# Kernel tuning notes

Measured on AMD Instinct MI355X. Metric: run time of the kernel, lower is better.

## Reference

```python
import jax, jax.numpy as jnp
import numpy as np
from jax.scipy.linalg import expm

ORDER = 256
SEQ_LEN = 4096
THETA = 4096.0
MEMORY_D = 4
INPUT_SIZE = 256
HIDDEN = 512
BATCH = 8


def _lmu_AB(order):
    # Continuous-time LMU (Legendre) state-space matrices
    q = np.arange(order, dtype=np.float64)
    r = 2.0 * q + 1.0
    i, j = np.meshgrid(q, q, indexing="ij")
    A = np.where(i < j, -1.0, (-1.0) ** (i - j + 1)) * r[:, None]
    B = ((-1.0) ** q * r)[:, None]
    return A, B


def _discretize_zoh(A, B, dt=1.0):
    # ZOH via augmented matrix exponential: expm([[A,B],[0,0]]*dt)
    n = A.shape[0]
    M = np.zeros((n + 1, n + 1))
    M[:n, :n] = A * dt
    M[:n, n:] = B * dt
    Md = expm(jnp.asarray(M, dtype=jnp.float64) if jax.config.jax_enable_x64 else jnp.asarray(M, dtype=jnp.float32))
    return Md[:n, :n].astype(jnp.float32), Md[:n, n:].astype(jnp.float32)


def _impulse_H(order, seq_len, theta):
    A, B = _lmu_AB(order)
    Ad, Bd = _discretize_zoh(A / theta, B / theta, 1.0)

    def step(A_i, _):
        # H_t = A^t B ; emit A_i @ Bd then advance A_i <- Ad @ A_i
        return Ad @ A_i, (A_i @ Bd)[:, 0]

    _, Hs = jax.lax.scan(step, jnp.eye(order, dtype=jnp.float32), None, length=seq_len)
    return Hs.T  # [order, seq_len]


def setup_inputs() -> dict:
    key = jax.random.key(0)
    k1, k2, k3, k4, k5 = jax.random.split(key, 5)
    x = jax.random.normal(k1, (BATCH, SEQ_LEN, INPUT_SIZE), dtype=jnp.float32)
    Wu_w = jax.random.normal(k2, (MEMORY_D, INPUT_SIZE), dtype=jnp.float32) * (1.0 / np.sqrt(INPUT_SIZE))
    Wu_b = jax.random.normal(k3, (MEMORY_D,), dtype=jnp.float32) * 0.01
    msz = MEMORY_D * ORDER + INPUT_SIZE
    Wh_w = jax.random.normal(k4, (HIDDEN, msz), dtype=jnp.float32) * (1.0 / np.sqrt(msz))
    Wh_b = jax.random.normal(k5, (HIDDEN,), dtype=jnp.float32) * 0.01
    H = _impulse_H(ORDER, SEQ_LEN, THETA)  # exact LMU impulse response buffer
    return {"x": x, "Wu_w": Wu_w, "Wu_b": Wu_b, "Wh_w": Wh_w, "Wh_b": Wh_b, "H": H}


def reference(x, Wu_w, Wu_b, Wh_w, Wh_b, H):
    B, L, _ = x.shape
    u = jax.nn.relu(x @ Wu_w.T + Wu_b)                     # [B, L, memory_d]
    fft_u = jnp.fft.rfft(u.transpose(0, 2, 1), n=2 * L, axis=-1)   # [B, md, L+1]
    fft_H = jnp.fft.rfft(H, n=2 * L, axis=-1)              # [order, L+1]
    temp = fft_u[:, :, None, :] * fft_H[None, None, :, :]  # [B, md, order, L+1]
    m = jnp.fft.irfft(temp, n=2 * L, axis=-1)[..., :L]     # [B, md, order, L]
    m = m.reshape(B, -1, L).transpose(0, 2, 1)             # [B, L, md*order]
    input_h = jnp.concatenate([m, x], axis=-1)             # [B, L, md*order + input]
    h = jax.nn.relu(input_h @ Wh_w.T + Wh_b)               # [B, L, hidden]
    return h, h[:, -1, :]
```

## Files before the change

kernel.cpp:

```cpp
#include <hip/hip_runtime.h>

#define NB 8
#define LSEQ 4096
#define INS 256
#define MD 4
#define ORD 256
#define HID 512
#define MSZ 1280
#define FS 4128
#define NSPEC 8256
#define GMT 1056768
#define GNT 16384

#define PD(n) ((n) + ((n) >> 3))
#define LDSN 4608

typedef __attribute__((ext_vector_type(8))) short short8;
typedef __attribute__((ext_vector_type(4))) float floatx4;

struct ush4 { unsigned short x, y, z, w; };

__device__ float2 g_tw4096[4096];
__device__ float2 g_tw8192[4098];

__device__ __forceinline__ unsigned short f2bf(float f) {
    unsigned u = __float_as_uint(f);
    u += 0x7FFF + ((u >> 16) & 1);
    return (unsigned short)(u >> 16);
}
__device__ __forceinline__ ush4 pack4(float4 v) {
    ush4 p; p.x = f2bf(v.x); p.y = f2bf(v.y); p.z = f2bf(v.z); p.w = f2bf(v.w); return p;
}
__device__ __forceinline__ float bf2f(unsigned short s) {
    return __uint_as_float(((unsigned)s) << 16);
}

__device__ __forceinline__ float2 cmul(float2 a, float2 b) {
    return make_float2(fmaf(a.x, b.x, -(a.y * b.y)), fmaf(a.x, b.y, a.y * b.x));
}
__device__ __forceinline__ float2 cadd(float2 a, float2 b) { return make_float2(a.x + b.x, a.y + b.y); }
__device__ __forceinline__ float2 csub(float2 a, float2 b) { return make_float2(a.x - b.x, a.y - b.y); }

template <int DIR>
__device__ __forceinline__ float2 jmul(float2 z) {
    return (DIR < 0) ? make_float2(z.y, -z.x) : make_float2(-z.y, z.x);
}

template <int DIR>
__device__ __forceinline__ void bfly8(const float2* a, float2* b) {
    const float2 e0 = cadd(a[0], a[4]), e1 = csub(a[0], a[4]);
    const float2 e2 = cadd(a[2], a[6]), e3 = jmul<DIR>(csub(a[2], a[6]));
    const float2 E0 = cadd(e0, e2), E2 = csub(e0, e2);
    const float2 E1 = cadd(e1, e3), E3 = csub(e1, e3);
    const float2 f0 = cadd(a[1], a[5]), f1 = csub(a[1], a[5]);
    const float2 f2 = cadd(a[3], a[7]), f3 = jmul<DIR>(csub(a[3], a[7]));
    const float2 O0 = cadd(f0, f2), O2 = csub(f0, f2);
    const float2 O1 = cadd(f1, f3), O3 = csub(f1, f3);
    constexpr float C707 = 0.70710678118654752440f;
    const float2 W1 = make_float2(C707, DIR * C707);
    const float2 W3 = make_float2(-C707, DIR * C707);
    const float2 T1 = cmul(O1, W1);
    const float2 T2 = jmul<DIR>(O2);
    const float2 T3 = cmul(O3, W3);
    b[0] = cadd(E0, O0); b[4] = csub(E0, O0);
    b[1] = cadd(E1, T1); b[5] = csub(E1, T1);
    b[2] = cadd(E2, T2); b[6] = csub(E2, T2);
    b[3] = cadd(E3, T3); b[7] = csub(E3, T3);
}

template <int DIR, int N_, int S_>
__device__ __forceinline__ void fft_stage_ip(float2* __restrict__ X, int tid) {
    constexpr int M_ = N_ / 8;
    constexpr int STEP = 4096 / N_;
    const int q = tid & (S_ - 1);
    const int p = tid / S_;
    const int rb = q + S_ * p;
    float2 a[8], b[8];
#pragma unroll
    for (int l = 0; l < 8; ++l) a[l] = X[PD(rb + S_ * l * M_)];

    const int pw = p * STEP;
    float2 w[7];
#pragma unroll
    for (int j = 1; j <= 7; ++j) {
        float2 t = g_tw4096[pw * j];
        if (DIR > 0) t.y = -t.y;
        w[j - 1] = t;
    }

    bfly8<DIR>(a, b);

    __syncthreads();

    const int wb = q + S_ * 8 * p;
    X[PD(wb + 0 * S_)] = b[0];
#pragma unroll
    for (int j = 1; j < 8; ++j)
        X[PD(wb + j * S_)] = cmul(b[j], w[j - 1]);
    __syncthreads();
}

extern "C" __global__ __launch_bounds__(256) void u_relu_k(
    const float* __restrict__ x, const float* __restrict__ Wuw,
    const float* __restrict__ Wub, float* __restrict__ u_t,
    unsigned short* __restrict__ x_bf,
    const float* __restrict__ Whw, unsigned short* __restrict__ Whw_bf,
    unsigned short* __restrict__ Wt) {
    const int blk = blockIdx.x;
    if (blk >= 8832) {
        if (blk < 8848) {
            const int i = (blk - 8832) * 256 + threadIdx.x;
            float sn, cs;
            sincosf(-1.53398078788564403e-3f * (float)i, &sn, &cs);
            g_tw4096[i] = make_float2(cs, sn);
        } else {
            const int i = (blk - 8848) * 256 + threadIdx.x;
            if (i <= 4097) {
                float sn, cs;
                sincosf(-7.66990393942820614e-4f * (float)i, &sn, &cs);
                g_tw8192[i] = make_float2(cs, sn);
            }
        }
        return;
    }
    if (blk >= 8704) {
        const int didx = (blk - 8704) * 1024 + threadIdx.x * 4;
        const int c = didx >> 14;
        const int r = didx & 16383;
        const int h = r >> 5, kk = r & 31;
        const float4 v = *(const float4*)(Whw + (size_t)h * MSZ + 1024 + c * 32 + kk);
        *(ush4*)(&Wt[didx]) = pack4(v);
        return;
    }
    if (blk >= 8192) {
        const int idx = (blk - 8192) * 256 + threadIdx.x;
        const int h = idx >> 8, c = idx & 255;
        const float4 v = ((const float4*)Whw)[(size_t)h * 320 + c];
        *(ush4*)(&Whw_bf[(size_t)idx * 4]) = pack4(v);
        return;
    }
    const int gid = blk * 256 + threadIdx.x;
    const int row = gid >> 6;
    const int lane = threadIdx.x & 63;
    const float4 xv = ((const float4*)x)[(size_t)row * 64 + lane];
    unsigned d0 = (unsigned)f2bf(xv.x) | ((unsigned)f2bf(xv.y) << 16);
    unsigned d1 = (unsigned)f2bf(xv.z) | ((unsigned)f2bf(xv.w) << 16);
    const unsigned e0 = (unsigned)__shfl_xor((int)d0, 1);
    const unsigned e1 = (unsigned)__shfl_xor((int)d1, 1);
    if (!(lane & 1)) {
        uint4 v; v.x = d0; v.y = d1; v.z = e0; v.w = e1;
        *(uint4*)(&x_bf[(size_t)row * 256 + lane * 4]) = v;
    }
    const float4 w0 = ((const float4*)Wuw)[0 * 64 + lane];
    const float4 w1 = ((const float4*)Wuw)[1 * 64 + lane];
    const float4 w2 = ((const float4*)Wuw)[2 * 64 + lane];
    const float4 w3 = ((const float4*)Wuw)[3 * 64 + lane];
    float a0 = xv.x * w0.x + xv.y * w0.y + xv.z * w0.z + xv.w * w0.w;
    float a1 = xv.x * w1.x + xv.y * w1.y + xv.z * w1.z + xv.w * w1.w;
    float a2 = xv.x * w2.x + xv.y * w2.y + xv.z * w2.z + xv.w * w2.w;
    float a3 = xv.x * w3.x + xv.y * w3.y + xv.z * w3.z + xv.w * w3.w;
#pragma unroll
    for (int off = 1; off < 64; off <<= 1) {
        a0 += __shfl_xor(a0, off);
        a1 += __shfl_xor(a1, off);
        a2 += __shfl_xor(a2, off);
        a3 += __shfl_xor(a3, off);
    }
    if (lane < 4) {
        float v = (lane == 0) ? a0 : (lane == 1) ? a1 : (lane == 2) ? a2 : a3;
        v = fmaxf(v + Wub[lane], 0.0f);
        const int b = row >> 12, t = row & 4095;
        u_t[((size_t)(b * 4 + lane)) * LSEQ + t] = v;
    }
}

extern "C" __global__ __launch_bounds__(512) void rfft_all_k(
    const float* __restrict__ ut, const float* __restrict__ H,
    float2* __restrict__ fftU, unsigned short* __restrict__ fftHB) {
    __shared__ float2 A[LDSN];
    const int blk = blockIdx.x;
    const int tid = threadIdx.x;
    const bool is_u = (blk < 32);
    const float* src = is_u ? (ut + (size_t)blk * LSEQ) : (H + (size_t)(blk - 32) * LSEQ);
    const float2* rp = (const float2*)src;
    {
        float2 c[8], b[8];
#pragma unroll
        for (int j = 0; j < 4; ++j) c[j] = rp[tid + j * 512];
#pragma unroll
        for (int j = 4; j < 8; ++j) c[j] = make_float2(0.f, 0.f);
        bfly8<-1>(c, b);
        A[PD(8 * tid + 0)] = b[0];
#pragma unroll
        for (int j = 1; j < 8; ++j)
            A[PD(8 * tid + j)] = cmul(b[j], g_tw4096[tid * j]);
    }
    __syncthreads();
    fft_stage_ip<-1, 512, 8>(A, tid);
    fft_stage_ip<-1, 64, 64>(A, tid);
    fft_stage_ip<-1, 8, 512>(A, tid);
    if (is_u) {
        float2* op = fftU + (size_t)blk * FS;
#pragma unroll
        for (int j = 0; j < 9; ++j) {
            const int k = tid + j * 512;
            if (k <= 4096) {
                const float2 Zk = A[PD(k & 4095)];
                const float2 Zm = A[PD((4096 - k) & 4095)];
                const float2 E = make_float2(0.5f * (Zk.x + Zm.x), 0.5f * (Zk.y - Zm.y));
                const float2 D = make_float2(0.5f * (Zk.x - Zm.x), 0.5f * (Zk.y + Zm.y));
                const float2 O = make_float2(D.y, -D.x);
                const float2 t = g_tw8192[k];
                op[k] = cadd(E, cmul(t, O));
            }
        }
    } else {
        const int o = blk - 32;
        unsigned* op = (unsigned*)(fftHB + (size_t)o * NSPEC);
#pragma unroll
        for (int j = 0; j < 9; ++j) {
            const int k = tid + j * 512;
            if (k <= 4096) {
                const float2 Zk = A[PD(k & 4095)];
                const float2 Zm = A[PD((4096 - k) & 4095)];
                const float2 E = make_float2(0.5f * (Zk.x + Zm.x), 0.5f * (Zk.y - Zm.y));
                const float2 D = make_float2(0.5f * (Zk.x - Zm.x), 0.5f * (Zk.y + Zm.y));
                const float2 O = make_float2(D.y, -D.x);
                const float2 t = g_tw8192[k];
                const float2 c = cadd(E, cmul(t, O));
                if (2 * k < NSPEC)
                    op[k] = (unsigned)f2bf(c.x) | ((unsigned)f2bf(c.y) << 16);
            }
        }
    }
}

extern "C" __global__ __launch_bounds__(256) void ht2_k(
    const unsigned short* __restrict__ fftHB, unsigned short* __restrict__ fftHT) {
    __shared__ unsigned short T[64 * 68];
    const int tid = threadIdx.x;
    const int s0 = blockIdx.x * 64;
    const int o0 = blockIdx.y * 64;
    const int r = tid >> 4, c4 = (tid & 15) * 4;
#pragma unroll
    for (int i = 0; i < 4; ++i) {
        const int o = r + 16 * i;
        const ush4 v = *(const ush4*)(fftHB + (size_t)(o0 + o) * NSPEC + s0 + c4);
        *(ush4*)(&T[o * 68 + c4]) = v;
    }
    __syncthreads();
#pragma unroll
    for (int i = 0; i < 4; ++i) {
        const int sl = r + 16 * i;
        const int s = s0 + sl;
        ush4 p;
        if (s < 8194) {
            p.x = T[(c4 + 0) * 68 + sl];
            p.y = T[(c4 + 1) * 68 + sl];
            p.z = T[(c4 + 2) * 68 + sl];
            p.w = T[(c4 + 3) * 68 + sl];
        } else { p.x = p.y = p.z = p.w = 0; }
        *(ush4*)(&fftHT[(size_t)s * 256 + o0 + c4]) = p;
    }
}

extern "C" __global__ __launch_bounds__(256) void g_gemm_k(
    const unsigned short* __restrict__ Whw_bf, const unsigned short* __restrict__ fftHT,
    unsigned short* __restrict__ fftG) {
    __shared__ __align__(16) char smem[36864];
    short* As = (short*)smem;
    short* Bs = (short*)(smem + 18432);
    short* Tt = (short*)smem;

    const int tid = threadIdx.x, lane = tid & 63, wave = tid >> 6;
    const int wg = blockIdx.x;
    const int loc = wg >> 3;
    const int mt = (wg & 7) * 2 + (loc & 1);
    const int nt = loc >> 1;
    const int m0 = mt * 128;
    const int n0 = nt * 128;
    floatx4 acc[2][8];
#pragma unroll
    for (int i = 0; i < 2; ++i)
#pragma unroll
        for (int j = 0; j < 8; ++j) acc[i][j] = (floatx4){0.f, 0.f, 0.f, 0.f};

    const int lr = tid >> 3;
    const int lc = (tid & 7) * 8;
    short8 ra[4], rb[4];

#define GL_A(kc, i) (*(const short8*)(Whw_bf + (size_t)((m0 + lr + 32 * (i)) >> 2) * 1024 + ((m0 + lr + 32 * (i)) & 3) * 256 + (kc) * 64 + lc))
#pragma unroll
    for (int i = 0; i < 4; ++i) {
        ra[i] = GL_A(0, i);
        const int n = n0 + lr + 32 * i;
        rb[i] = (n < NSPEC) ? *(const short8*)(fftHT + (size_t)n * 256 + lc)
                            : (short8){0, 0, 0, 0, 0, 0, 0, 0};
    }

    for (int kc = 0; kc < 4; ++kc) {
#pragma unroll
        for (int i = 0; i < 4; ++i) {
            *(short8*)(&As[(lr + 32 * i) * 72 + lc]) = ra[i];
            *(short8*)(&Bs[(lr + 32 * i) * 72 + lc]) = rb[i];
        }
        __syncthreads();
        if (kc < 3) {
#pragma unroll
            for (int i = 0; i < 4; ++i) {
                ra[i] = GL_A(kc + 1, i);
                const int n = n0 + lr + 32 * i;
                rb[i] = (n < NSPEC) ? *(const short8*)(fftHT + (size_t)n * 256 + (kc + 1) * 64 + lc)
                                    : (short8){0, 0, 0, 0, 0, 0, 0, 0};
            }
        }
        const int arow = (wave * 32 + (lane & 15)) * 72;
        const int brow = (lane & 15) * 72;
        const int kq = 8 * (lane >> 4);
#pragma unroll
        for (int kk = 0; kk < 2; ++kk) {
            const int ko = kk * 32 + kq;
            const short8 a0 = *(const short8*)(&As[arow + ko]);
            const short8 a1 = *(const short8*)(&As[arow + 16 * 72 + ko]);
#pragma unroll
            for (int nf = 0; nf < 8; ++nf) {
                const short8 bv = *(const short8*)(&Bs[brow + nf * 16 * 72 + ko]);
                acc[0][nf] = __builtin_amdgcn_mfma_f32_16x16x32_bf16(a0, bv, acc[0][nf], 0, 0, 0);
                acc[1][nf] = __builtin_amdgcn_mfma_f32_16x16x32_bf16(a1, bv, acc[1][nf], 0, 0, 0);
            }
        }
        __syncthreads();
    }
#undef GL_A
    const int wm = wave * 32;
#pragma unroll
    for (int mf = 0; mf < 2; ++mf) {
        const int row = wm + mf * 16 + 4 * (lane >> 4);
#pragma unroll
        for (int nf = 0; nf < 8; ++nf) {
            const int col = nf * 16 + (lane & 15);
#pragma unroll
            for (int r = 0; r < 4; ++r)
                Tt[(row + r) * 136 + col] = (short)f2bf(acc[mf][nf][r]);
        }
    }
    __syncthreads();
    const size_t gb = (size_t)mt * GMT + (size_t)nt * GNT;
    if (n0 < 8192) {
#pragma unroll
        for (int i = 0; i < 8; ++i) {
            const int idx = tid + i * 256;
            const int ml = idx >> 4, c8 = (idx & 15) * 8;
            const short8 v = *(const short8*)(&Tt[ml * 136 + c8]);
            *(short8*)(&fftG[gb + (size_t)idx * 8]) = v;
        }
    } else {
#pragma unroll
        for (int i = 0; i < 4; ++i) {
            const int idx = tid + i * 256;
            const int ml = idx >> 3, c8 = (idx & 7) * 8;
            const short8 v = *(const short8*)(&Tt[ml * 136 + c8]);
            *(short8*)(&fftG[gb + (size_t)idx * 8]) = v;
        }
    }
}

extern "C" __global__ __launch_bounds__(512) void conv_ifft_k(
    const float2* __restrict__ fftU, const unsigned short* __restrict__ fftG,
    unsigned short* __restrict__ y) {
    __shared__ float2 A[LDSN];
    __shared__ float2 S4096;
    const int wg = blockIdx.x;
    const int h = ((wg & 7) << 6) + (wg >> 6);
    const int b = (wg >> 3) & 7;
    const int tid = threadIdx.x;
    const float2* U = fftU + (size_t)b * MD * FS;
    const size_t mbase = (size_t)(h >> 5) * GMT + (size_t)((h & 31) * 4) * 128;
    const size_t tail = (size_t)(h >> 5) * GMT + (size_t)64 * GNT + (size_t)((h & 31) * 4) * 64;
#pragma unroll
    for (int j = 0; j < 9; ++j) {
        const int k = tid + j * 512;
        if (k <= 4096) {
            float2 s = make_float2(0.f, 0.f);
#pragma unroll
            for (int d = 0; d < MD; ++d) {
                const unsigned gv = (k < 4096)
                    ? *(const unsigned*)(fftG + mbase + (size_t)d * 128 + (size_t)(k >> 6) * GNT + (k & 63) * 2)
                    : *(const unsigned*)(fftG + tail + (size_t)d * 64);
                const float2 uu = U[d * FS + k];
                const float gx = __uint_as_float(gv << 16);
                const float gy = __uint_as_float(gv & 0xFFFF0000u);
                s.x = fmaf(uu.x, gx, fmaf(-uu.y, gy, s.x));
                s.y = fmaf(uu.x, gy, fmaf(uu.y, gx, s.y));
            }
            if (k < 4096) A[PD(k)] = s;
            else S4096 = s;
        }
    }
    __syncthreads();
    float2 c[8], bt[8];
#pragma unroll
    for (int j = 0; j < 8; ++j) {
        const int k = tid + j * 512;
        const float2 Sk = A[PD(k)];
        const float2 Sm = (k == 0) ? S4096 : A[PD(4096 - k)];
        const float2 E = make_float2(0.5f * (Sk.x + Sm.x), 0.5f * (Sk.y - Sm.y));
        const float2 D = make_float2(0.5f * (Sk.x - Sm.x), 0.5f * (Sk.y + Sm.y));
        const float2 t = g_tw8192[k];
        const float2 tc = make_float2(t.x, -t.y);
        const float2 O = cmul(D, tc);
        c[j] = make_float2(E.x - O.y, E.y + O.x);
    }
    __syncthreads();
    bfly8<1>(c, bt);
    A[PD(8 * tid + 0)] = bt[0];
#pragma unroll
    for (int j = 1; j < 8; ++j) {
        float2 t = g_tw4096[tid * j]; t.y = -t.y;
        A[PD(8 * tid + j)] = cmul(bt[j], t);
    }
    __syncthreads();
    fft_stage_ip<1, 512, 8>(A, tid);
    fft_stage_ip<1, 64, 64>(A, tid);
    {
        float2 z[8], bo[8];
#pragma unroll
        for (int k = 0; k < 8; ++k) z[k] = A[PD(tid + 512 * k)];
        bfly8<1>(z, bo);
        const float inv = 1.0f / 4096.0f;
#pragma unroll
        for (int k = 0; k < 4; ++k)
            A[PD(tid + 512 * k)] = make_float2(bo[k].x * inv, bo[k].y * inv);
    }
    __syncthreads();
    unsigned short* yp = y + (size_t)(b * HID + h) * LSEQ;
    {
        const int q = tid;
        unsigned dw[4];
#pragma unroll
        for (int jj = 0; jj < 4; ++jj) {
            const float2 z = A[PD(4 * q + jj)];
            dw[jj] = (unsigned)f2bf(z.x) | ((unsigned)f2bf(z.y) << 16);
        }
        uint4 v; v.x = dw[0]; v.y = dw[1]; v.z = dw[2]; v.w = dw[3];
        *(uint4*)(yp + 8 * q) = v;
    }
}

extern "C" __global__ __launch_bounds__(256) void out_gemm_k(
    const unsigned short* __restrict__ x_bf, const unsigned short* __restrict__ Wt,
    const float* __restrict__ Whb, const unsigned short* __restrict__ y,
    float* __restrict__ out) {
    __shared__ __align__(16) char smem[66560];
    short* As = (short*)smem;
    short* Bs = (short*)(smem + 2560);
    float* Whbs = (float*)smem;
    short* Ys = (short*)(smem + 2560);
    float* Ct = (float*)smem;

    const int tid = threadIdx.x, lane = tid & 63, wave = tid >> 6;
    const int wg = blockIdx.x;
    const int s = ((wg & 7) << 7) + (wg >> 3);
    const int m0 = s * 32;
    const int b = m0 >> 12;
    const int t0 = m0 & 4095;
    const int hq = wave * 128;

    floatx4 acc[2][8];
#pragma unroll
    for (int i = 0; i < 2; ++i)
#pragma unroll
        for (int j = 0; j < 8; ++j) acc[i][j] = (floatx4){0.f, 0.f, 0.f, 0.f};

    short8 ra, rb[8];
    const int arow = tid >> 2, acb = (tid & 3) * 8;
    if (tid < 128) ra = *(const short8*)(x_bf + (size_t)(m0 + arow) * INS + acb);
#pragma unroll
    for (int j = 0; j < 8; ++j)
        rb[j] = *(const short8*)(Wt + (size_t)tid * 64 + j * 8);

    for (int c = 0; c < 8; ++c) {
        if (tid < 128) *(short8*)(&As[arow * 40 + acb]) = ra;
#pragma unroll
        for (int j = 0; j < 8; ++j)
            *(short8*)(&Bs[(2 * tid + (j >> 2)) * 40 + (j & 3) * 8]) = rb[j];
        __syncthreads();
        if (c < 7) {
            if (tid < 128) ra = *(const short8*)(x_bf + (size_t)(m0 + arow) * INS + (c + 1) * 32 + acb);
#pragma unroll
            for (int j = 0; j < 8; ++j)
                rb[j] = *(const short8*)(Wt + (size_t)(c + 1) * 16384 + (size_t)tid * 64 + j * 8);
        }
        const int kq = 8 * (lane >> 4);
        const short8 a0 = *(const short8*)(&As[(lane & 15) * 40 + kq]);
        const short8 a1 = *(const short8*)(&As[((lane & 15) + 16) * 40 + kq]);
#pragma unroll
        for (int nf = 0; nf < 8; ++nf) {
            const short8 bv = *(const short8*)(&Bs[(hq + nf * 16 + (lane & 15)) * 40 + kq]);
            acc[0][nf] = __builtin_amdgcn_mfma_f32_16x16x32_bf16(a0, bv, acc[0][nf], 0, 0, 0);
            acc[1][nf] = __builtin_amdgcn_mfma_f32_16x16x32_bf16(a1, bv, acc[1][nf], 0, 0, 0);
        }
        __syncthreads();
    }

    Whbs[tid] = Whb[tid];
    Whbs[tid + 256] = Whb[tid + 256];
#pragma unroll
    for (int i = 0; i < 16; ++i) {
        const int idx = tid + i * 256;
        const int hh = idx >> 3, tq = (idx & 7) * 4;
        const ush4 v = *(const ush4*)(y + (size_t)(b * HID + hh) * LSEQ + t0 + tq);
        *(ush4*)(&Ys[hh * 36 + tq]) = v;
    }
    __syncthreads();
#pragma unroll
    for (int nf = 0; nf < 8; ++nf) {
        const int hh = hq + nf * 16 + (lane & 15);
        const float bias = Whbs[hh];
#pragma unroll
        for (int mf = 0; mf < 2; ++mf)
#pragma unroll
            for (int r = 0; r < 4; ++r) {
                const int row = mf * 16 + 4 * (lane >> 4) + r;
                acc[mf][nf][r] = fmaxf(acc[mf][nf][r] + bf2f(Ys[hh * 36 + row]) + bias, 0.f);
            }
    }
    __syncthreads();
#pragma unroll
    for (int nf = 0; nf < 8; ++nf) {
        const int col = hq + nf * 16 + (lane & 15);
#pragma unroll
        for (int mf = 0; mf < 2; ++mf)
#pragma unroll
            for (int r = 0; r < 4; ++r) {
                const int row = mf * 16 + 4 * (lane >> 4) + r;
                Ct[row * 520 + col] = acc[mf][nf][r];
            }
    }
    __syncthreads();
#pragma unroll
    for (int i = 0; i < 16; ++i) {
        const int idx = tid + i * 256;
        const int row = idx >> 7, c4 = (idx & 127) * 4;
        const floatx4 t = *(const floatx4*)&Ct[row * 520 + c4];
        *(floatx4*)(out + (size_t)(m0 + row) * HID + c4) = t;
        if (((m0 + row) & 4095) == 4095)
            *(floatx4*)(out + (size_t)NB * LSEQ * HID + (size_t)b * HID + c4) = t;
    }
}

extern "C" void kernel_launch(void* const* d_in, const int* in_sizes, int n_in,
                              void* d_out, int out_size, void* d_ws, size_t ws_size,
                              hipStream_t stream) {
    const float* x   = (const float*)d_in[0];
    const float* Wuw = (const float*)d_in[1];
    const float* Wub = (const float*)d_in[2];
    const float* Whw = (const float*)d_in[3];
    const float* Whb = (const float*)d_in[4];
    const float* H   = (const float*)d_in[5];
    char* wsb = (char*)d_ws;
    unsigned short* fftG   = (unsigned short*)(wsb);
    unsigned short* yb     = (unsigned short*)(wsb + 33816576);
    float*          fftU   = (float*)(wsb + 67371008);
    unsigned short* fftHT  = (unsigned short*)(wsb + 68427776);
    float*          ut     = (float*)(wsb + 72654848);
    unsigned short* x_bf   = (unsigned short*)(wsb + 73179136);
    unsigned short* Whw_bf = (unsigned short*)(wsb + 89956352);
    unsigned short* Wt     = (unsigned short*)(wsb + 91004928);
    unsigned short* fftHB  = (unsigned short*)(wsb + 91267072);
    float* out = (float*)d_out;

    hipLaunchKernelGGL(u_relu_k, dim3(8865), dim3(256), 0, stream, x, Wuw, Wub, ut, x_bf, Whw, Whw_bf, Wt);
    hipLaunchKernelGGL(rfft_all_k, dim3(288), dim3(512), 0, stream, ut, H, (float2*)fftU, fftHB);
    hipLaunchKernelGGL(ht2_k, dim3(129, 4), dim3(256), 0, stream, fftHB, fftHT);
    hipLaunchKernelGGL(g_gemm_k, dim3(1040), dim3(256), 0, stream, Whw_bf, fftHT, fftG);
    hipLaunchKernelGGL(conv_ifft_k, dim3(4096), dim3(512), 0, stream,
                       (const float2*)fftU, fftG, yb);
    hipLaunchKernelGGL(out_gemm_k, dim3(1024), dim3(256), 0, stream, x_bf, Wt, Whb, yb, out);
}
```

Measured before the change: 245.5 us.

## Shrink LDS footprint in output GEMM and FFT padding to raise occupancy

The output GEMM epilogue now reads the y residual and bias straight from global memory into registers instead of staging them in LDS. The C tile is written back in two column halves so it fits in a 260-wide buffer, which cuts the kernel's shared memory from about 65 KB to 38 KB. The A/B tile row stride drops from 40 to 36 shorts, and the FFT padding changes from one slot per 8 elements to one per 32, which shrinks that LDS buffer too. The aim is more resident workgroups per CU, at the cost of possible new LDS bank conflicts, extra barriers, and uncoalesced 8-byte global loads of y.

```diff
diff --git a/kernel.cpp b/kernel.cpp
--- a/kernel.cpp
+++ b/kernel.cpp
@@ -12,8 +12,8 @@
 #define GMT 1056768
 #define GNT 16384
 
-#define PD(n) ((n) + ((n) >> 3))
-#define LDSN 4608
+#define PD(n) ((n) + ((n) >> 5))
+#define LDSN 4224
 
 typedef __attribute__((ext_vector_type(8))) short short8;
 typedef __attribute__((ext_vector_type(4))) float floatx4;
@@ -451,11 +451,9 @@
     const unsigned short* __restrict__ x_bf, const unsigned short* __restrict__ Wt,
     const float* __restrict__ Whb, const unsigned short* __restrict__ y,
     float* __restrict__ out) {
-    __shared__ __align__(16) char smem[66560];
+    __shared__ __align__(16) char smem[39168];
     short* As = (short*)smem;
-    short* Bs = (short*)(smem + 2560);
-    float* Whbs = (float*)smem;
-    short* Ys = (short*)(smem + 2560);
+    short* Bs = (short*)(smem + 2304);
     float* Ct = (float*)smem;
 
     const int tid = threadIdx.x, lane = tid & 63, wave = tid >> 6;
@@ -480,10 +478,10 @@
         rb[j] = *(const short8*)(Wt + (size_t)tid * 64 + j * 8);
 
     for (int c = 0; c < 8; ++c) {
-        if (tid < 128) *(short8*)(&As[arow * 40 + acb]) = ra;
+        if (tid < 128) *(short8*)(&As[arow * 36 + acb]) = ra;
 #pragma unroll
         for (int j = 0; j < 8; ++j)
-            *(short8*)(&Bs[(2 * tid + (j >> 2)) * 40 + (j & 3) * 8]) = rb[j];
+            *(short8*)(&Bs[(2 * tid + (j >> 2)) * 36 + (j & 3) * 8]) = rb[j];
         __syncthreads();
         if (c < 7) {
             if (tid < 128) ra = *(const short8*)(x_bf + (size_t)(m0 + arow) * INS + (c + 1) * 32 + acb);
@@ -492,60 +490,64 @@
                 rb[j] = *(const short8*)(Wt + (size_t)(c + 1) * 16384 + (size_t)tid * 64 + j * 8);
         }
         const int kq = 8 * (lane >> 4);
-        const short8 a0 = *(const short8*)(&As[(lane & 15) * 40 + kq]);
-        const short8 a1 = *(const short8*)(&As[((lane & 15) + 16) * 40 + kq]);
+        const short8 a0 = *(const short8*)(&As[(lane & 15) * 36 + kq]);
+        const short8 a1 = *(const short8*)(&As[((lane & 15) + 16) * 36 + kq]);
 #pragma unroll
         for (int nf = 0; nf < 8; ++nf) {
-            const short8 bv = *(const short8*)(&Bs[(hq + nf * 16 + (lane & 15)) * 40 + kq]);
+            const short8 bv = *(const short8*)(&Bs[(hq + nf * 16 + (lane & 15)) * 36 + kq]);
             acc[0][nf] = __builtin_amdgcn_mfma_f32_16x16x32_bf16(a0, bv, acc[0][nf], 0, 0, 0);
             acc[1][nf] = __builtin_amdgcn_mfma_f32_16x16x32_bf16(a1, bv, acc[1][nf], 0, 0, 0);
         }
         __syncthreads();
     }
 
-    Whbs[tid] = Whb[tid];
-    Whbs[tid + 256] = Whb[tid + 256];
-#pragma unroll
-    for (int i = 0; i < 16; ++i) {
-        const int idx = tid + i * 256;
-        const int hh = idx >> 3, tq = (idx & 7) * 4;
-        const ush4 v = *(const ush4*)(y + (size_t)(b * HID + hh) * LSEQ + t0 + tq);
-        *(ush4*)(&Ys[hh * 36 + tq]) = v;
-    }
-    __syncthreads();
+    ush4 yv[8][2];
+    float bias[8];
 #pragma unroll
     for (int nf = 0; nf < 8; ++nf) {
         const int hh = hq + nf * 16 + (lane & 15);
-        const float bias = Whbs[hh];
 #pragma unroll
         for (int mf = 0; mf < 2; ++mf)
-#pragma unroll
-            for (int r = 0; r < 4; ++r) {
-                const int row = mf * 16 + 4 * (lane >> 4) + r;
-                acc[mf][nf][r] = fmaxf(acc[mf][nf][r] + bf2f(Ys[hh * 36 + row]) + bias, 0.f);
-            }
-    }
-    __syncthreads();
-#pragma unroll
-    for (int nf = 0; nf < 8; ++nf) {
-        const int col = hq + nf * 16 + (lane & 15);
-#pragma unroll
-        for (int mf = 0; mf < 2; ++mf)
-#pragma unroll
-            for (int r = 0; r < 4; ++r) {
-                const int row = mf * 16 + 4 * (lane >> 4) + r;
-                Ct[row * 520 + col] = acc[mf][nf][r];
-            }
-    }
-    __syncthreads();
-#pragma unroll
-    for (int i = 0; i < 16; ++i) {
-        const int idx = tid + i * 256;
-        const int row = idx >> 7, c4 = (idx & 127) * 4;
-        const floatx4 t = *(const floatx4*)&Ct[row * 520 + c4];
-        *(floatx4*)(out + (size_t)(m0 + row) * HID + c4) = t;
-        if (((m0 + row) & 4095) == 4095)
-            *(floatx4*)(out + (size_t)NB * LSEQ * HID + (size_t)b * HID + c4) = t;
+            yv[nf][mf] = *(const ush4*)(y + (size_t)(b * HID + hh) * LSEQ + t0 + mf * 16 + 4 * (lane >> 4));
+        bias[nf] = Whb[hh];
+    }
+#pragma unroll
+    for (int nf = 0; nf < 8; ++nf)
+#pragma unroll
+        for (int mf = 0; mf < 2; ++mf) {
+            acc[mf][nf][0] = fmaxf(acc[mf][nf][0] + bf2f(yv[nf][mf].x) + bias[nf], 0.f);
+            acc[mf][nf][1] = fmaxf(acc[mf][nf][1] + bf2f(yv[nf][mf].y) + bias[nf], 0.f);
+            acc[mf][nf][2] = fmaxf(acc[mf][nf][2] + bf2f(yv[nf][mf].z) + bias[nf], 0.f);
+            acc[mf][nf][3] = fmaxf(acc[mf][nf][3] + bf2f(yv[nf][mf].w) + bias[nf], 0.f);
+        }
+
+#pragma unroll 1
+    for (int half = 0; half < 2; ++half) {
+        __syncthreads();
+        if ((wave >> 1) == half) {
+            const int cb = hq & 255;
+#pragma unroll
+            for (int nf = 0; nf < 8; ++nf) {
+                const int col = cb + nf * 16 + (lane & 15);
+#pragma unroll
+                for (int mf = 0; mf < 2; ++mf)
+#pragma unroll
+                    for (int r = 0; r < 4; ++r) {
+                        const int row = mf * 16 + 4 * (lane >> 4) + r;
+                        Ct[row * 260 + col] = acc[mf][nf][r];
+                    }
+            }
+        }
+        __syncthreads();
+#pragma unroll
+        for (int i = 0; i < 8; ++i) {
+            const int idx = tid + i * 256;
+            const int row = idx >> 6, c4 = (idx & 63) * 4;
+            const floatx4 t = *(const floatx4*)&Ct[row * 260 + c4];
+            *(floatx4*)(out + (size_t)(m0 + row) * HID + half * 256 + c4) = t;
+            if (((m0 + row) & 4095) == 4095)
+                *(floatx4*)(out + (size_t)NB * LSEQ * HID + (size_t)b * HID + half * 256 + c4) = t;
+        }
     }
 }
 
```

After: 266.0 us. 8.4% more time.

## Regroup preprocessing kernels to co-schedule independent H FFT with projection work

Applied to the files above, without the earlier changes.

Splits the preprocessing pipeline into a small weight/twiddle prep kernel, a stage that runs the H FFTs alongside the x projection and bf16 cast, and a stage that runs the u FFTs alongside the H spectrum transpose. Independent work now shares kernels, which removes serialization between the small u FFT grid and the transpose and lets the 32 u FFT blocks run concurrently with other work. It also lowers LDS padding from every 8 to every 32 elements, cutting shared memory per block, and skips the unit twiddle multiply in the last radix-8 stage. The lighter padding may add bank conflicts. Each H FFT block now depends on twiddles written by an earlier launch, so the prep kernel must finish before stage 1 runs.

```diff
diff --git a/kernel.cpp b/kernel.cpp
--- a/kernel.cpp
+++ b/kernel.cpp
@@ -12,8 +12,8 @@
 #define GMT 1056768
 #define GNT 16384
 
-#define PD(n) ((n) + ((n) >> 3))
-#define LDSN 4608
+#define PD(n) ((n) + ((n) >> 5))
+#define LDSN 4224
 
 typedef __attribute__((ext_vector_type(8))) short short8;
 typedef __attribute__((ext_vector_type(4))) float floatx4;
@@ -79,13 +79,15 @@
 #pragma unroll
     for (int l = 0; l < 8; ++l) a[l] = X[PD(rb + S_ * l * M_)];
 
-    const int pw = p * STEP;
     float2 w[7];
-#pragma unroll
-    for (int j = 1; j <= 7; ++j) {
-        float2 t = g_tw4096[pw * j];
-        if (DIR > 0) t.y = -t.y;
-        w[j - 1] = t;
+    if constexpr (N_ != 8) {
+        const int pw = p * STEP;
+#pragma unroll
+        for (int j = 1; j <= 7; ++j) {
+            float2 t = g_tw4096[pw * j];
+            if (DIR > 0) t.y = -t.y;
+            w[j - 1] = t;
+        }
     }
 
     bfly8<DIR>(a, b);
@@ -93,129 +95,77 @@
     __syncthreads();
 
     const int wb = q + S_ * 8 * p;
-    X[PD(wb + 0 * S_)] = b[0];
-#pragma unroll
-    for (int j = 1; j < 8; ++j)
-        X[PD(wb + j * S_)] = cmul(b[j], w[j - 1]);
-    __syncthreads();
-}
-
-extern "C" __global__ __launch_bounds__(256) void u_relu_k(
-    const float* __restrict__ x, const float* __restrict__ Wuw,
-    const float* __restrict__ Wub, float* __restrict__ u_t,
-    unsigned short* __restrict__ x_bf,
+    if constexpr (N_ == 8) {
+#pragma unroll
+        for (int j = 0; j < 8; ++j)
+            X[PD(wb + j * S_)] = b[j];
+    } else {
+        X[PD(wb + 0 * S_)] = b[0];
+#pragma unroll
+        for (int j = 1; j < 8; ++j)
+            X[PD(wb + j * S_)] = cmul(b[j], w[j - 1]);
+    }
+    __syncthreads();
+}
+
+extern "C" __global__ __launch_bounds__(256) void prep_k(
     const float* __restrict__ Whw, unsigned short* __restrict__ Whw_bf,
     unsigned short* __restrict__ Wt) {
     const int blk = blockIdx.x;
-    if (blk >= 8832) {
-        if (blk < 8848) {
-            const int i = (blk - 8832) * 256 + threadIdx.x;
-            float sn, cs;
-            sincosf(-1.53398078788564403e-3f * (float)i, &sn, &cs);
-            g_tw4096[i] = make_float2(cs, sn);
-        } else {
-            const int i = (blk - 8848) * 256 + threadIdx.x;
-            if (i <= 4097) {
-                float sn, cs;
-                sincosf(-7.66990393942820614e-4f * (float)i, &sn, &cs);
-                g_tw8192[i] = make_float2(cs, sn);
-            }
-        }
-        return;
-    }
-    if (blk >= 8704) {
-        const int didx = (blk - 8704) * 1024 + threadIdx.x * 4;
+    if (blk < 512) {
+        const int idx = blk * 256 + threadIdx.x;
+        const int h = idx >> 8, c = idx & 255;
+        const float4 v = ((const float4*)Whw)[(size_t)h * 320 + c];
+        *(ush4*)(&Whw_bf[(size_t)idx * 4]) = pack4(v);
+    } else if (blk < 640) {
+        const int didx = (blk - 512) * 1024 + threadIdx.x * 4;
         const int c = didx >> 14;
         const int r = didx & 16383;
         const int h = r >> 5, kk = r & 31;
         const float4 v = *(const float4*)(Whw + (size_t)h * MSZ + 1024 + c * 32 + kk);
         *(ush4*)(&Wt[didx]) = pack4(v);
-        return;
-    }
-    if (blk >= 8192) {
-        const int idx = (blk - 8192) * 256 + threadIdx.x;
-        const int h = idx >> 8, c = idx & 255;
-        const float4 v = ((const float4*)Whw)[(size_t)h * 320 + c];
-        *(ush4*)(&Whw_bf[(size_t)idx * 4]) = pack4(v);
-        return;
-    }
-    const int gid = blk * 256 + threadIdx.x;
-    const int row = gid >> 6;
-    const int lane = threadIdx.x & 63;
-    const float4 xv = ((const float4*)x)[(size_t)row * 64 + lane];
-    unsigned d0 = (unsigned)f2bf(xv.x) | ((unsigned)f2bf(xv.y) << 16);
-    unsigned d1 = (unsigned)f2bf(xv.z) | ((unsigned)f2bf(xv.w) << 16);
-    const unsigned e0 = (unsigned)__shfl_xor((int)d0, 1);
-    const unsigned e1 = (unsigned)__shfl_xor((int)d1, 1);
-    if (!(lane & 1)) {
-        uint4 v; v.x = d0; v.y = d1; v.z = e0; v.w = e1;
-        *(uint4*)(&x_bf[(size_t)row * 256 + lane * 4]) = v;
-    }
-    const float4 w0 = ((const float4*)Wuw)[0 * 64 + lane];
-    const float4 w1 = ((const float4*)Wuw)[1 * 64 + lane];
-    const float4 w2 = ((const float4*)Wuw)[2 * 64 + lane];
-    const float4 w3 = ((const float4*)Wuw)[3 * 64 + lane];
-    float a0 = xv.x * w0.x + xv.y * w0.y + xv.z * w0.z + xv.w * w0.w;
-    float a1 = xv.x * w1.x + xv.y * w1.y + xv.z * w1.z + xv.w * w1.w;
-    float a2 = xv.x * w2.x + xv.y * w2.y + xv.z * w2.z + xv.w * w2.w;
-    float a3 = xv.x * w3.x + xv.y * w3.y + xv.z * w3.z + xv.w * w3.w;
-#pragma unroll
-    for (int off = 1; off < 64; off <<= 1) {
-        a0 += __shfl_xor(a0, off);
-        a1 += __shfl_xor(a1, off);
-        a2 += __shfl_xor(a2, off);
-        a3 += __shfl_xor(a3, off);
-    }
-    if (lane < 4) {
-        float v = (lane == 0) ? a0 : (lane == 1) ? a1 : (lane == 2) ? a2 : a3;
-        v = fmaxf(v + Wub[lane], 0.0f);
-        const int b = row >> 12, t = row & 4095;
-        u_t[((size_t)(b * 4 + lane)) * LSEQ + t] = v;
-    }
-}
-
-extern "C" __global__ __launch_bounds__(512) void rfft_all_k(
-    const float* __restrict__ ut, const float* __restrict__ H,
-    float2* __restrict__ fftU, unsigned short* __restrict__ fftHB) {
-    __shared__ float2 A[LDSN];
+    } else if (blk < 656) {
+        const int i = (blk - 640) * 256 + threadIdx.x;
+        float sn, cs;
+        sincosf(-1.53398078788564403e-3f * (float)i, &sn, &cs);
+        g_tw4096[i] = make_float2(cs, sn);
+    } else {
+        const int i = (blk - 656) * 256 + threadIdx.x;
+        if (i <= 4097) {
+            float sn, cs;
+            sincosf(-7.66990393942820614e-4f * (float)i, &sn, &cs);
+            g_tw8192[i] = make_float2(cs, sn);
+        }
+    }
+}
+
+extern "C" __global__ __launch_bounds__(512) void stage1_k(
+    const float* __restrict__ x, const float* __restrict__ Wuw,
+    const float* __restrict__ Wub, float* __restrict__ u_t,
+    unsigned short* __restrict__ x_bf,
+    const float* __restrict__ H, unsigned short* __restrict__ fftHB) {
     const int blk = blockIdx.x;
     const int tid = threadIdx.x;
-    const bool is_u = (blk < 32);
-    const float* src = is_u ? (ut + (size_t)blk * LSEQ) : (H + (size_t)(blk - 32) * LSEQ);
-    const float2* rp = (const float2*)src;
-    {
-        float2 c[8], b[8];
-#pragma unroll
-        for (int j = 0; j < 4; ++j) c[j] = rp[tid + j * 512];
-#pragma unroll
-        for (int j = 4; j < 8; ++j) c[j] = make_float2(0.f, 0.f);
-        bfly8<-1>(c, b);
-        A[PD(8 * tid + 0)] = b[0];
-#pragma unroll
-        for (int j = 1; j < 8; ++j)
-            A[PD(8 * tid + j)] = cmul(b[j], g_tw4096[tid * j]);
-    }
-    __syncthreads();
-    fft_stage_ip<-1, 512, 8>(A, tid);
-    fft_stage_ip<-1, 64, 64>(A, tid);
-    fft_stage_ip<-1, 8, 512>(A, tid);
-    if (is_u) {
-        float2* op = fftU + (size_t)blk * FS;
-#pragma unroll
-        for (int j = 0; j < 9; ++j) {
-            const int k = tid + j * 512;
-            if (k <= 4096) {
-                const float2 Zk = A[PD(k & 4095)];
-                const float2 Zm = A[PD((4096 - k) & 4095)];
-                const float2 E = make_float2(0.5f * (Zk.x + Zm.x), 0.5f * (Zk.y - Zm.y));
-                const float2 D = make_float2(0.5f * (Zk.x - Zm.x), 0.5f * (Zk.y + Zm.y));
-                const float2 O = make_float2(D.y, -D.x);
-                const float2 t = g_tw8192[k];
-                op[k] = cadd(E, cmul(t, O));
-            }
-        }
-    } else {
-        const int o = blk - 32;
+    if (blk < 256) {
+        __shared__ float2 A[LDSN];
+        const int o = blk;
+        const float2* rp = (const float2*)(H + (size_t)o * LSEQ);
+        {
+            float2 c[8], b[8];
+#pragma unroll
+            for (int j = 0; j < 4; ++j) c[j] = rp[tid + j * 512];
+#pragma unroll
+            for (int j = 4; j < 8; ++j) c[j] = make_float2(0.f, 0.f);
+            bfly8<-1>(c, b);
+            A[PD(8 * tid + 0)] = b[0];
+#pragma unroll
+            for (int j = 1; j < 8; ++j)
+                A[PD(8 * tid + j)] = cmul(b[j], g_tw4096[tid * j]);
+        }
+        __syncthreads();
+        fft_stage_ip<-1, 512, 8>(A, tid);
+        fft_stage_ip<-1, 64, 64>(A, tid);
+        fft_stage_ip<-1, 8, 512>(A, tid);
         unsigned* op = (unsigned*)(fftHB + (size_t)o * NSPEC);
 #pragma unroll
         for (int j = 0; j < 9; ++j) {
@@ -232,21 +182,94 @@
                     op[k] = (unsigned)f2bf(c.x) | ((unsigned)f2bf(c.y) << 16);
             }
         }
-    }
-}
-
-extern "C" __global__ __launch_bounds__(256) void ht2_k(
+        return;
+    }
+    const int row = (blk - 256) * 8 + (tid >> 6);
+    const int lane = tid & 63;
+    const float4 xv = ((const float4*)x)[(size_t)row * 64 + lane];
+    unsigned d0 = (unsigned)f2bf(xv.x) | ((unsigned)f2bf(xv.y) << 16);
+    unsigned d1 = (unsigned)f2bf(xv.z) | ((unsigned)f2bf(xv.w) << 16);
+    const unsigned e0 = (unsigned)__shfl_xor((int)d0, 1);
+    const unsigned e1 = (unsigned)__shfl_xor((int)d1, 1);
+    if (!(lane & 1)) {
+        uint4 v; v.x = d0; v.y = d1; v.z = e0; v.w = e1;
+        *(uint4*)(&x_bf[(size_t)row * 256 + lane * 4]) = v;
+    }
+    const float4 w0 = ((const float4*)Wuw)[0 * 64 + lane];
+    const float4 w1 = ((const float4*)Wuw)[1 * 64 + lane];
+    const float4 w2 = ((const float4*)Wuw)[2 * 64 + lane];
+    const float4 w3 = ((const float4*)Wuw)[3 * 64 + lane];
+    float a0 = xv.x * w0.x + xv.y * w0.y + xv.z * w0.z + xv.w * w0.w;
+    float a1 = xv.x * w1.x + xv.y * w1.y + xv.z * w1.z + xv.w * w1.w;
+    float a2 = xv.x * w2.x + xv.y * w2.y + xv.z * w2.z + xv.w * w2.w;
+    float a3 = xv.x * w3.x + xv.y * w3.y + xv.z * w3.z + xv.w * w3.w;
+#pragma unroll
+    for (int off = 1; off < 64; off <<= 1) {
+        a0 += __shfl_xor(a0, off);
+        a1 += __shfl_xor(a1, off);
+        a2 += __shfl_xor(a2, off);
+        a3 += __shfl_xor(a3, off);
+    }
+    if (lane < 4) {
+        float v = (lane == 0) ? a0 : (lane == 1) ? a1 : (lane == 2) ? a2 : a3;
+        v = fmaxf(v + Wub[lane], 0.0f);
+        const int b = row >> 12, t = row & 4095;
+        u_t[((size_t)(b * 4 + lane)) * LSEQ + t] = v;
+    }
+}
+
+extern "C" __global__ __launch_bounds__(512) void stage2_k(
+    const float* __restrict__ ut, float2* __restrict__ fftU,
     const unsigned short* __restrict__ fftHB, unsigned short* __restrict__ fftHT) {
-    __shared__ unsigned short T[64 * 68];
+    const int blk = blockIdx.x;
     const int tid = threadIdx.x;
-    const int s0 = blockIdx.x * 64;
-    const int o0 = blockIdx.y * 64;
-    const int r = tid >> 4, c4 = (tid & 15) * 4;
+    if (blk < 32) {
+        __shared__ float2 A[LDSN];
+        const float2* rp = (const float2*)(ut + (size_t)blk * LSEQ);
+        {
+            float2 c[8], b[8];
+#pragma unroll
+            for (int j = 0; j < 4; ++j) c[j] = rp[tid + j * 512];
+#pragma unroll
+            for (int j = 4; j < 8; ++j) c[j] = make_float2(0.f, 0.f);
+            bfly8<-1>(c, b);
+            A[PD(8 * tid + 0)] = b[0];
+#pragma unroll
+            for (int j = 1; j < 8; ++j)
+                A[PD(8 * tid + j)] = cmul(b[j], g_tw4096[tid * j]);
+        }
+        __syncthreads();
+        fft_stage_ip<-1, 512, 8>(A, tid);
+        fft_stage_ip<-1, 64, 64>(A, tid);
+        fft_stage_ip<-1, 8, 512>(A, tid);
+        float2* op = fftU + (size_t)blk * FS;
+#pragma unroll
+        for (int j = 0; j < 9; ++j) {
+            const int k = tid + j * 512;
+            if (k <= 4096) {
+                const float2 Zk = A[PD(k & 4095)];
+                const float2 Zm = A[PD((4096 - k) & 4095)];
+                const float2 E = make_float2(0.5f * (Zk.x + Zm.x), 0.5f * (Zk.y - Zm.y));
+                const float2 D = make_float2(0.5f * (Zk.x - Zm.x), 0.5f * (Zk.y + Zm.y));
+                const float2 O = make_float2(D.y, -D.x);
+                const float2 t = g_tw8192[k];
+                op[k] = cadd(E, cmul(t, O));
+            }
+        }
+        return;
+    }
+    __shared__ unsigned short T[2][64 * 68];
+    const int sub = tid >> 8;
+    const int tt = tid & 255;
+    const int t = (blk - 32) * 2 + sub;
+    const int s0 = (t % 129) * 64;
+    const int o0 = (t / 129) * 64;
+    const int r = tt >> 4, c4 = (tt & 15) * 4;
 #pragma unroll
     for (int i = 0; i < 4; ++i) {
         const int o = r + 16 * i;
         const ush4 v = *(const ush4*)(fftHB + (size_t)(o0 + o) * NSPEC + s0 + c4);
-        *(ush4*)(&T[o * 68 + c4]) = v;
+        *(ush4*)(&T[sub][o * 68 + c4]) = v;
     }
     __syncthreads();
 #pragma unroll
@@ -255,10 +278,10 @@
         const int s = s0 + sl;
         ush4 p;
         if (s < 8194) {
-            p.x = T[(c4 + 0) * 68 + sl];
-            p.y = T[(c4 + 1) * 68 + sl];
-            p.z = T[(c4 + 2) * 68 + sl];
-            p.w = T[(c4 + 3) * 68 + sl];
+            p.x = T[sub][(c4 + 0) * 68 + sl];
+            p.y = T[sub][(c4 + 1) * 68 + sl];
+            p.z = T[sub][(c4 + 2) * 68 + sl];
+            p.w = T[sub][(c4 + 3) * 68 + sl];
         } else { p.x = p.y = p.z = p.w = 0; }
         *(ush4*)(&fftHT[(size_t)s * 256 + o0 + c4]) = p;
     }
@@ -561,7 +584,7 @@
     char* wsb = (char*)d_ws;
     unsigned short* fftG   = (unsigned short*)(wsb);
     unsigned short* yb     = (unsigned short*)(wsb + 33816576);
-    float*          fftU   = (float*)(wsb + 67371008);
+    float2*         fftU   = (float2*)(wsb + 67371008);
     unsigned short* fftHT  = (unsigned short*)(wsb + 68427776);
     float*          ut     = (float*)(wsb + 72654848);
     unsigned short* x_bf   = (unsigned short*)(wsb + 73179136);
@@ -570,11 +593,10 @@
     unsigned short* fftHB  = (unsigned short*)(wsb + 91267072);
     float* out = (float*)d_out;
 
-    hipLaunchKernelGGL(u_relu_k, dim3(8865), dim3(256), 0, stream, x, Wuw, Wub, ut, x_bf, Whw, Whw_bf, Wt);
-    hipLaunchKernelGGL(rfft_all_k, dim3(288), dim3(512), 0, stream, ut, H, (float2*)fftU, fftHB);
-    hipLaunchKernelGGL(ht2_k, dim3(129, 4), dim3(256), 0, stream, fftHB, fftHT);
+    hipLaunchKernelGGL(prep_k, dim3(673), dim3(256), 0, stream, Whw, Whw_bf, Wt);
+    hipLaunchKernelGGL(stage1_k, dim3(4352), dim3(512), 0, stream, x, Wuw, Wub, ut, x_bf, H, fftHB);
+    hipLaunchKernelGGL(stage2_k, dim3(290), dim3(512), 0, stream, ut, fftU, fftHB, fftHT);
     hipLaunchKernelGGL(g_gemm_k, dim3(1040), dim3(256), 0, stream, Whw_bf, fftHT, fftG);
-    hipLaunchKernelGGL(conv_ifft_k, dim3(4096), dim3(512), 0, stream,
-                       (const float2*)fftU, fftG, yb);
+    hipLaunchKernelGGL(conv_ifft_k, dim3(4096), dim3(512), 0, stream, fftU, fftG, yb);
     hipLaunchKernelGGL(out_gemm_k, dim3(1024), dim3(256), 0, stream, x_bf, Wt, Whb, yb, out);
 }
```

Result: no change. 247.7 us (median of 2 runs) (+0.9%).
